# Kernel tuning notes

Hardware: AMD Instinct MI355X
Metric: run time of the kernel (lower is better)

## Reference

```python
import jax, jax.numpy as jnp
import numpy as np

B, L, D, K, MAXL = 2, 1024, 256, 64, 1024
EPS = 1e-5

def _encode(x, pos, w1, b1, w2, b2, wa, ba):
    # x: [B,L,D] -> complex phasors [B,L,K]
    xa = x + pos[: x.shape[1]][None]
    h = jax.nn.gelu(xa @ w1 + b1, approximate=False)
    phase = jnp.tanh(h @ w2 + b2) * np.float32(np.pi)
    amp = jax.nn.softplus(xa @ wa + ba) + np.float32(0.1)
    return (amp * jnp.exp(1j * phase)).astype(jnp.complex64)

def setup_inputs() -> dict:
    key = jax.random.key(0)
    ks = jax.random.split(key, 24)
    def lin_w(k, i, o):
        return (jax.random.normal(k, (i, o), jnp.float32) / np.sqrt(np.float32(i)))
    def pos(k):
        return jax.random.normal(k, (MAXL, D), jnp.float32) * np.float32(0.02)
    inp = {
        'x': jax.random.normal(ks[0], (B, L, D), jnp.float32),
        'pos_k': pos(ks[1]),
        'w1_k': lin_w(ks[2], D, D), 'b1_k': jnp.zeros((D,), jnp.float32),
        'w2_k': lin_w(ks[3], D, K), 'b2_k': jnp.zeros((K,), jnp.float32),
        'wa_k': lin_w(ks[4], D, K), 'ba_k': jnp.zeros((K,), jnp.float32),
        'pos_q': pos(ks[5]),
        'w1_q': lin_w(ks[6], D, D), 'b1_q': jnp.zeros((D,), jnp.float32),
        'w2_q': lin_w(ks[7], D, K), 'b2_q': jnp.zeros((K,), jnp.float32),
        'wa_q': lin_w(ks[8], D, K), 'ba_q': jnp.zeros((K,), jnp.float32),
        'wv': lin_w(ks[9], D, D), 'bv': jnp.zeros((D,), jnp.float32),
        'ln_g': jnp.ones((D,), jnp.float32), 'ln_b': jnp.zeros((D,), jnp.float32),
        'wo': lin_w(ks[10], D, D), 'bo': jnp.zeros((D,), jnp.float32),
    }
    return inp

def reference(x, pos_k, w1_k, b1_k, w2_k, b2_k, wa_k, ba_k,
              pos_q, w1_q, b1_q, w2_q, b2_q, wa_q, ba_q,
              wv, bv, ln_g, ln_b, wo, bo):
    Bx, Lx, Dx = x.shape
    kp = _encode(x, pos_k, w1_k, b1_k, w2_k, b2_k, wa_k, ba_k)  # [B,L,K] complex
    qp = _encode(x, pos_q, w1_q, b1_q, w2_q, b2_q, wa_q, ba_q)  # [B,L,K] complex
    V = (x @ wv + bv).astype(jnp.complex64)                      # [B,L,D]
    bound = kp[:, :, :, None] * V[:, :, None, :]                 # [B,L,K,D]
    memory = jnp.cumsum(bound, axis=1)                           # [B,L,K,D]
    retrieved = jnp.real(jnp.einsum('blkd,blk->bld', memory, jnp.conj(qp)))
    positions = jnp.arange(1, Lx + 1, dtype=jnp.float32)
    norm = jnp.sqrt(positions * np.float32(kp.shape[-1]))[None, :, None]
    r = retrieved / norm
    mu = jnp.mean(r, axis=-1, keepdims=True)
    var = jnp.var(r, axis=-1, keepdims=True)
    rn = (r - mu) / jnp.sqrt(var + np.float32(EPS)) * ln_g + ln_b
    return x + rn @ wo + bo
```

## Files before the change

### kernel.cpp

```cpp
#include <hip/hip_runtime.h>
#include <hip/hip_bf16.h>

typedef __attribute__((ext_vector_type(8))) short short8;
typedef __attribute__((ext_vector_type(4))) float float4v;

constexpr int B = 2, L = 1024, D = 256, K = 64;
constexpr int N = B * L;
constexpr int NC = L / 64;

constexpr int WT2_OFF = 524288;

__device__ __forceinline__ ushort bf16_hi(float v) {
  return (ushort)(__float_as_uint(v) >> 16);
}
__device__ __forceinline__ float hi_f(float v) {
  return __uint_as_float(__float_as_uint(v) & 0xFFFF0000u);
}
__device__ __forceinline__ ushort bf16_rne(float v) {
  uint b = __float_as_uint(v);
  b += 0x7FFF + ((b >> 16) & 1);
  return (ushort)(b >> 16);
}

__global__ __launch_bounds__(256) void prep_kernel(
    const float* __restrict__ w1_k, const float* __restrict__ w1_q,
    const float* __restrict__ wv, const float* __restrict__ wo,
    const float* __restrict__ w2_k, const float* __restrict__ wa_k,
    const float* __restrict__ w2_q, const float* __restrict__ wa_q,
    ushort* __restrict__ WT) {
  __shared__ float Lt[64][65];
  const int bi = blockIdx.x, tid = threadIdx.x;
  const float* src;
  int ncols, k0, n0;
  ushort* dhi;
  int losz;
  if (bi < 64) {
    const int m = bi >> 4, t = bi & 15;
    src = (m == 0) ? w1_k : (m == 1) ? w1_q : (m == 2) ? wv : wo;
    ncols = 256; k0 = (t >> 2) * 64; n0 = (t & 3) * 64;
    dhi = WT + m * 131072; losz = 65536;
  } else {
    const int m = (bi - 64) >> 2, kt = (bi - 64) & 3;
    src = (m == 0) ? w2_k : (m == 1) ? wa_k : (m == 2) ? w2_q : wa_q;
    ncols = 64; k0 = kt * 64; n0 = 0;
    dhi = WT + WT2_OFF + m * 32768; losz = 16384;
  }
  ushort* dlo = dhi + losz;
  for (int p = 0; p < 16; ++p) {
    const int kr = p * 4 + (tid >> 6), nc = tid & 63;
    Lt[kr][nc] = src[(k0 + kr) * ncols + n0 + nc];
  }
  __syncthreads();
  const int n = tid >> 2, kq = tid & 3;
  uint uh[8], ul[8];
  for (int i = 0; i < 8; ++i) {
    const float v0 = Lt[kq * 16 + 2 * i][n];
    const float v1 = Lt[kq * 16 + 2 * i + 1][n];
    uh[i] = (uint)bf16_hi(v0) | ((uint)bf16_hi(v1) << 16);
    ul[i] = (uint)bf16_rne(v0 - hi_f(v0)) | ((uint)bf16_rne(v1 - hi_f(v1)) << 16);
  }
  const int oidx = (n0 + n) * 256 + k0 + kq * 16;
  *(uint4*)&dhi[oidx] = make_uint4(uh[0], uh[1], uh[2], uh[3]);
  *(uint4*)&dhi[oidx + 8] = make_uint4(uh[4], uh[5], uh[6], uh[7]);
  *(uint4*)&dlo[oidx] = make_uint4(ul[0], ul[1], ul[2], ul[3]);
  *(uint4*)&dlo[oidx + 8] = make_uint4(ul[4], ul[5], ul[6], ul[7]);
}

__global__ __launch_bounds__(256) void enc1_kernel(
    const float* __restrict__ x, const float* __restrict__ pos_k,
    const float* __restrict__ pos_q,
    const float* __restrict__ b1_k, const float* __restrict__ b1_q,
    const float* __restrict__ bv, const ushort* __restrict__ WT,
    float* __restrict__ hk, float* __restrict__ hq, float* __restrict__ V) {
  __shared__ __align__(16) ushort Ah[32][40], Al[32][40];
  __shared__ __align__(16) ushort Bh[128][40], Bl[128][40];
  const int tid = threadIdx.x;
  const int g = blockIdx.x / 128;
  const int rem = blockIdx.x % 128;
  const int row0 = (rem >> 1) * 32, nb = (rem & 1) * 128;
  const float* pos = (g == 0) ? pos_k : (g == 1) ? pos_q : nullptr;
  const ushort* Wh = WT + g * 131072;
  const ushort* Wl = Wh + 65536;
  const int w = tid >> 6, lane = tid & 63;
  const int m16 = lane & 15, quad = lane >> 4;

  float4v acc[2][2] = {};

  for (int k0 = 0; k0 < 256; k0 += 32) {
    __syncthreads();
    {
      const int r = tid >> 3, kc = (tid & 7) * 4;
      const int row = row0 + r, l = row & (L - 1);
      float4 xv = *(const float4*)&x[row * D + k0 + kc];
      if (pos) {
        const float4 pv = *(const float4*)&pos[l * D + k0 + kc];
        xv.x += pv.x; xv.y += pv.y; xv.z += pv.z; xv.w += pv.w;
      }
      ushort4 h4, l4;
      h4.x = bf16_hi(xv.x); l4.x = bf16_rne(xv.x - hi_f(xv.x));
      h4.y = bf16_hi(xv.y); l4.y = bf16_rne(xv.y - hi_f(xv.y));
      h4.z = bf16_hi(xv.z); l4.z = bf16_rne(xv.z - hi_f(xv.z));
      h4.w = bf16_hi(xv.w); l4.w = bf16_rne(xv.w - hi_f(xv.w));
      *(ushort4*)&Ah[r][kc] = h4;
      *(ushort4*)&Al[r][kc] = l4;
    }
#pragma unroll
    for (int p = 0; p < 2; ++p) {
      const int n = (tid >> 2) + p * 64, chunk = tid & 3;
      const int ga = (nb + n) * 256 + k0 + chunk * 8;
      *(uint4*)&Bh[n][chunk * 8] = *(const uint4*)&Wh[ga];
      *(uint4*)&Bl[n][chunk * 8] = *(const uint4*)&Wl[ga];
    }
    __syncthreads();

    short8 afh[2], afl[2], bfh[2], bfl[2];
#pragma unroll
    for (int r = 0; r < 2; ++r) {
      afh[r] = *(const short8*)&Ah[r * 16 + m16][quad * 8];
      afl[r] = *(const short8*)&Al[r * 16 + m16][quad * 8];
    }
#pragma unroll
    for (int c = 0; c < 2; ++c) {
      const int col = w * 32 + c * 16 + m16;
      bfh[c] = *(const short8*)&Bh[col][quad * 8];
      bfl[c] = *(const short8*)&Bl[col][quad * 8];
    }
#pragma unroll
    for (int r = 0; r < 2; ++r)
#pragma unroll
      for (int c = 0; c < 2; ++c) {
        acc[r][c] = __builtin_amdgcn_mfma_f32_16x16x32_bf16(afh[r], bfh[c], acc[r][c], 0, 0, 0);
        acc[r][c] = __builtin_amdgcn_mfma_f32_16x16x32_bf16(afh[r], bfl[c], acc[r][c], 0, 0, 0);
        acc[r][c] = __builtin_amdgcn_mfma_f32_16x16x32_bf16(afl[r], bfh[c], acc[r][c], 0, 0, 0);
      }
  }

  float* outp = (g == 0) ? hk : (g == 1) ? hq : V;
  const float* bp = (g == 0) ? b1_k : (g == 1) ? b1_q : bv;
#pragma unroll
  for (int c = 0; c < 2; ++c) {
    const int colg = nb + w * 32 + c * 16 + m16;
    const float bias = bp[colg];
#pragma unroll
    for (int r = 0; r < 2; ++r)
#pragma unroll
      for (int j = 0; j < 4; ++j) {
        const int rowg = row0 + r * 16 + quad * 4 + j;
        float v = acc[r][c][j] + bias;
        if (g < 2) v = 0.5f * v * (1.0f + erff(v * 0.70710678f));
        outp[rowg * D + colg] = v;
      }
  }
}

__global__ __launch_bounds__(256) void enc2_kernel(
    const float* __restrict__ x, const float* __restrict__ pos_k,
    const float* __restrict__ pos_q, const float* __restrict__ hk,
    const float* __restrict__ hq,
    const float* __restrict__ b2_k, const float* __restrict__ ba_k,
    const float* __restrict__ b2_q, const float* __restrict__ ba_q,
    const ushort* __restrict__ WT,
    float* __restrict__ kr, float* __restrict__ ki,
    float* __restrict__ qr, float* __restrict__ qi) {
  __shared__ __align__(16) ushort Ahh[16][40], Ahl[16][40], Axh[16][40], Axl[16][40];
  __shared__ __align__(16) ushort B2h[64][40], B2l[64][40], Bah[64][40], Bal[64][40];
  const int tid = threadIdx.x;
  const int e = blockIdx.x >> 7;
  const int r0g = (blockIdx.x & 127) * 16;
  const float* hsrc = e ? hq : hk;
  const float* pos = e ? pos_q : pos_k;
  const ushort* W2h = WT + WT2_OFF + (e ? 2 : 0) * 32768;
  const ushort* W2l = W2h + 16384;
  const ushort* Wah = WT + WT2_OFF + (e ? 3 : 1) * 32768;
  const ushort* Wal = Wah + 16384;
  const int w = tid >> 6, lane = tid & 63;
  const int m16 = lane & 15, quad = lane >> 4;

  float4v accP = {}, accA = {};
  for (int k0 = 0; k0 < 256; k0 += 32) {
    __syncthreads();
    {
      const int r = tid >> 4, kc = (tid & 15) * 2;
      const int row = r0g + r, l = row & (L - 1);
      const float2 hv = *(const float2*)&hsrc[row * D + k0 + kc];
      const float2 xv = *(const float2*)&x[row * D + k0 + kc];
      const float2 pv = *(const float2*)&pos[l * D + k0 + kc];
      const float a0 = xv.x + pv.x, a1 = xv.y + pv.y;
      ushort2 t;
      t.x = bf16_hi(hv.x); t.y = bf16_hi(hv.y); *(ushort2*)&Ahh[r][kc] = t;
      t.x = bf16_rne(hv.x - hi_f(hv.x)); t.y = bf16_rne(hv.y - hi_f(hv.y));
      *(ushort2*)&Ahl[r][kc] = t;
      t.x = bf16_hi(a0); t.y = bf16_hi(a1); *(ushort2*)&Axh[r][kc] = t;
      t.x = bf16_rne(a0 - hi_f(a0)); t.y = bf16_rne(a1 - hi_f(a1));
      *(ushort2*)&Axl[r][kc] = t;
    }
    {
      const int n = tid >> 2, chunk = tid & 3;
      const int ga = n * 256 + k0 + chunk * 8;
      *(uint4*)&B2h[n][chunk * 8] = *(const uint4*)&W2h[ga];
      *(uint4*)&B2l[n][chunk * 8] = *(const uint4*)&W2l[ga];
      *(uint4*)&Bah[n][chunk * 8] = *(const uint4*)&Wah[ga];
      *(uint4*)&Bal[n][chunk * 8] = *(const uint4*)&Wal[ga];
    }
    __syncthreads();

    const short8 ahh = *(const short8*)&Ahh[m16][quad * 8];
    const short8 ahl = *(const short8*)&Ahl[m16][quad * 8];
    const short8 axh = *(const short8*)&Axh[m16][quad * 8];
    const short8 axl = *(const short8*)&Axl[m16][quad * 8];
    const int col = w * 16 + m16;
    const short8 b2h = *(const short8*)&B2h[col][quad * 8];
    const short8 b2l = *(const short8*)&B2l[col][quad * 8];
    const short8 bah = *(const short8*)&Bah[col][quad * 8];
    const short8 bal = *(const short8*)&Bal[col][quad * 8];
    accP = __builtin_amdgcn_mfma_f32_16x16x32_bf16(ahh, b2h, accP, 0, 0, 0);
    accP = __builtin_amdgcn_mfma_f32_16x16x32_bf16(ahh, b2l, accP, 0, 0, 0);
    accP = __builtin_amdgcn_mfma_f32_16x16x32_bf16(ahl, b2h, accP, 0, 0, 0);
    accA = __builtin_amdgcn_mfma_f32_16x16x32_bf16(axh, bah, accA, 0, 0, 0);
    accA = __builtin_amdgcn_mfma_f32_16x16x32_bf16(axh, bal, accA, 0, 0, 0);
    accA = __builtin_amdgcn_mfma_f32_16x16x32_bf16(axl, bah, accA, 0, 0, 0);
  }

  float* pr = e ? qr : kr;
  float* pim = e ? qi : ki;
  const float* b2 = e ? b2_q : b2_k;
  const float* ba = e ? ba_q : ba_k;
  const int colk = w * 16 + m16;
  const float b2v = b2[colk], bav = ba[colk];
#pragma unroll
  for (int j = 0; j < 4; ++j) {
    const int row = r0g + quad * 4 + j;
    const float ph = tanhf(accP[j] + b2v) * 3.14159265358979f;
    const float av = accA[j] + bav;
    const float am = fmaxf(av, 0.0f) + log1pf(expf(-fabsf(av))) + 0.1f;
    pr[row * K + colk] = am * cosf(ph);
    pim[row * K + colk] = am * sinf(ph);
  }
}

__global__ __launch_bounds__(256) void tbuild_kernel(
    const float* __restrict__ kr, const float* __restrict__ ki,
    const float* __restrict__ V, float* __restrict__ TMt) {
  const int id = blockIdx.x;
  const int dc = id & 15, c = (id >> 4) & 15, b = id >> 8;
  const int tid = threadIdx.x;
  const int n0 = b * L + c * 64;
  const int dl = tid & 15;
  const int d = dc * 16 + dl;
  const int kb = tid >> 4;

  __shared__ float krL[64][68], kiL[64][68];
  __shared__ float Tl[16][200];
  for (int e = tid; e < 1024; e += 256) {
    const int t = e >> 4, k4 = (e & 15) * 4;
    *(float4*)&krL[t][k4] = *(const float4*)&kr[(n0 + t) * K + k4];
    *(float4*)&kiL[t][k4] = *(const float4*)&ki[(n0 + t) * K + k4];
  }
  __syncthreads();

  float vcol[64];
#pragma unroll 8
  for (int t = 0; t < 64; ++t) vcol[t] = V[(n0 + t) * D + d];

  float ar[4] = {0.f, 0.f, 0.f, 0.f}, ai[4] = {0.f, 0.f, 0.f, 0.f};
#pragma unroll 4
  for (int t = 0; t < 64; ++t) {
    const float vt = vcol[t];
    const float4 k4r = *(const float4*)&krL[t][kb * 4];
    const float4 k4i = *(const float4*)&kiL[t][kb * 4];
    ar[0] += k4r.x * vt; ar[1] += k4r.y * vt; ar[2] += k4r.z * vt; ar[3] += k4r.w * vt;
    ai[0] += k4i.x * vt; ai[1] += k4i.y * vt; ai[2] += k4i.z * vt; ai[3] += k4i.w * vt;
  }

#pragma unroll
  for (int i = 0; i < 4; ++i) {
    Tl[dl][kb * 4 + i] = ar[i];
    Tl[dl][64 + kb * 4 + i] = ai[i];
  }
  if (kb == 0) {
#pragma unroll
    for (int j = 0; j < 16; ++j) Tl[dl][128 + j] = vcol[j];
  } else if (kb == 1) {
#pragma unroll
    for (int j = 0; j < 16; ++j) Tl[dl][144 + j] = vcol[16 + j];
  } else if (kb == 2) {
#pragma unroll
    for (int j = 0; j < 16; ++j) Tl[dl][160 + j] = vcol[32 + j];
  } else if (kb == 3) {
#pragma unroll
    for (int j = 0; j < 16; ++j) Tl[dl][176 + j] = vcol[48 + j];
  }
  __syncthreads();

  float* dst = &TMt[(((size_t)(b * 16 + c)) * 256 + dc * 16) * 192];
#pragma unroll
  for (int p = 0; p < 3; ++p) {
    const int e = p * 256 + tid;
    const int row = e / 48, f4 = e % 48;
    *(float4*)&dst[(size_t)row * 192 + f4 * 4] = *(const float4*)&Tl[row][f4 * 4];
  }
}

__global__ __launch_bounds__(256) void scan_kernel(float* __restrict__ TMt) {
  const int col = blockIdx.x * 256 + threadIdx.x;
  const int b = col >> 15;
  const int d = (col >> 7) & 255;
  const int inner = col & 127;
  size_t idx = (((size_t)(b * 16)) * 256 + d) * 192 + inner;
  const size_t stride = (size_t)256 * 192;
  float run = 0.f;
#pragma unroll
  for (int c = 0; c < NC; ++c, idx += stride) {
    const float t = TMt[idx];
    TMt[idx] = run;
    run += t;
  }
}

__global__ __launch_bounds__(256) void ret_kernel(
    const float* __restrict__ qr, const float* __restrict__ qi,
    const float* __restrict__ kr, const float* __restrict__ ki,
    const float* __restrict__ TMt, float* __restrict__ ret,
    float* __restrict__ LNred) {
  __shared__ __align__(16) ushort Ah[64][200], Al[64][200];
  __shared__ __align__(16) ushort Kh[64][136], Kl[64][136];
  __shared__ __align__(16) ushort Bh[32][200], Bl[32][200];
  const int tid = threadIdx.x;
  const int dc = blockIdx.x & 7;
  const int c = (blockIdx.x >> 3) & 15;
  const int b = blockIdx.x >> 7;
  const int n0 = b * L + c * 64;
  const int cols0 = dc * 32;
  const int w = tid >> 6, lane = tid & 63;
  const int m16 = lane & 15, quad = lane >> 4;

#pragma unroll
  for (int j = 0; j < 8; ++j) {
    const int e = j * 256 + tid;
    const int row = e >> 5, c4 = e & 31;
    const int col0 = (c4 & 15) * 4;
    const int acol = (c4 < 16 ? 0 : 64) + col0;
    {
      const float* src = (c4 < 16) ? qr : qi;
      const float4 v = *(const float4*)&src[(n0 + row) * K + col0];
      ushort4 h4, l4;
      h4.x = bf16_hi(v.x); l4.x = bf16_rne(v.x - hi_f(v.x));
      h4.y = bf16_hi(v.y); l4.y = bf16_rne(v.y - hi_f(v.y));
      h4.z = bf16_hi(v.z); l4.z = bf16_rne(v.z - hi_f(v.z));
      h4.w = bf16_hi(v.w); l4.w = bf16_rne(v.w - hi_f(v.w));
      *(ushort4*)&Ah[row][acol] = h4;
      *(ushort4*)&Al[row][acol] = l4;
    }
    {
      const float* src = (c4 < 16) ? kr : ki;
      const float4 v = *(const float4*)&src[(n0 + row) * K + col0];
      ushort4 h4, l4;
      h4.x = bf16_hi(v.x); l4.x = bf16_rne(v.x - hi_f(v.x));
      h4.y = bf16_hi(v.y); l4.y = bf16_rne(v.y - hi_f(v.y));
      h4.z = bf16_hi(v.z); l4.z = bf16_rne(v.z - hi_f(v.z));
      h4.w = bf16_hi(v.w); l4.w = bf16_rne(v.w - hi_f(v.w));
      *(ushort4*)&Kh[row][acol] = h4;
      *(ushort4*)&Kl[row][acol] = l4;
    }
  }
  __syncthreads();

  {
    float4v sc[4] = {};
#pragma unroll
    for (int kk = 0; kk < 128; kk += 32) {
      const short8 ah = *(const short8*)&Ah[w * 16 + m16][kk + quad * 8];
      const short8 al = *(const short8*)&Al[w * 16 + m16][kk + quad * 8];
#pragma unroll
      for (int ct = 0; ct < 4; ++ct) {
        const short8 bh = *(const short8*)&Kh[ct * 16 + m16][kk + quad * 8];
        const short8 bl = *(const short8*)&Kl[ct * 16 + m16][kk + quad * 8];
        sc[ct] = __builtin_amdgcn_mfma_f32_16x16x32_bf16(ah, bh, sc[ct], 0, 0, 0);
        sc[ct] = __builtin_amdgcn_mfma_f32_16x16x32_bf16(ah, bl, sc[ct], 0, 0, 0);
        sc[ct] = __builtin_amdgcn_mfma_f32_16x16x32_bf16(al, bh, sc[ct], 0, 0, 0);
      }
    }
#pragma unroll
    for (int ct = 0; ct < 4; ++ct)
#pragma unroll
      for (int j = 0; j < 4; ++j) {
        const int row = w * 16 + quad * 4 + j;
        const int t = ct * 16 + m16;
        const float s = (t <= row) ? sc[ct][j] : 0.0f;
        Ah[row][128 + t] = bf16_hi(s);
        Al[row][128 + t] = bf16_rne(s - hi_f(s));
      }
  }

  {
    const float* src = &TMt[(((size_t)(b * 16 + c)) * 256 + cols0) * 192];
#pragma unroll
    for (int p = 0; p < 6; ++p) {
      const int e = p * 256 + tid;
      const int row = e / 48, f4 = e % 48;
      const float4 v = *(const float4*)&src[(size_t)row * 192 + f4 * 4];
      ushort4 h4, l4;
      h4.x = bf16_hi(v.x); l4.x = bf16_rne(v.x - hi_f(v.x));
      h4.y = bf16_hi(v.y); l4.y = bf16_rne(v.y - hi_f(v.y));
      h4.z = bf16_hi(v.z); l4.z = bf16_rne(v.z - hi_f(v.z));
      h4.w = bf16_hi(v.w); l4.w = bf16_rne(v.w - hi_f(v.w));
      *(ushort4*)&Bh[row][f4 * 4] = h4;
      *(ushort4*)&Bl[row][f4 * 4] = l4;
    }
  }
  __syncthreads();

  {
    float4v r2[2] = {};
#pragma unroll
    for (int kk = 0; kk < 6; ++kk) {
      const short8 ah = *(const short8*)&Ah[w * 16 + m16][kk * 32 + quad * 8];
      const short8 al = *(const short8*)&Al[w * 16 + m16][kk * 32 + quad * 8];
#pragma unroll
      for (int ct = 0; ct < 2; ++ct) {
        const short8 bh = *(const short8*)&Bh[ct * 16 + m16][kk * 32 + quad * 8];
        const short8 bl = *(const short8*)&Bl[ct * 16 + m16][kk * 32 + quad * 8];
        r2[ct] = __builtin_amdgcn_mfma_f32_16x16x32_bf16(ah, bh, r2[ct], 0, 0, 0);
        r2[ct] = __builtin_amdgcn_mfma_f32_16x16x32_bf16(ah, bl, r2[ct], 0, 0, 0);
        r2[ct] = __builtin_amdgcn_mfma_f32_16x16x32_bf16(al, bh, r2[ct], 0, 0, 0);
      }
    }
#pragma unroll
    for (int j = 0; j < 4; ++j) {
      const int rowL = w * 16 + quad * 4 + j;
      const float nrm = rsqrtf((float)(c * 64 + rowL + 1) * 64.0f);
      float sj = 0.f, s2j = 0.f;
#pragma unroll
      for (int ct = 0; ct < 2; ++ct) {
        const float v = r2[ct][j] * nrm;
        ret[(size_t)(n0 + rowL) * D + cols0 + ct * 16 + m16] = v;
        sj += v; s2j += v * v;
      }
      for (int off = 1; off < 16; off <<= 1) {
        sj += __shfl_xor(sj, off, 64);
        s2j += __shfl_xor(s2j, off, 64);
      }
      if (m16 == 0) {
        LNred[(size_t)(n0 + rowL) * 16 + dc * 2 + 0] = sj;
        LNred[(size_t)(n0 + rowL) * 16 + dc * 2 + 1] = s2j;
      }
    }
  }
}

__global__ __launch_bounds__(256) void out2_kernel(
    const float* __restrict__ ret, const float* __restrict__ LNred,
    const float* __restrict__ x, const float* __restrict__ ln_g,
    const float* __restrict__ ln_b, const ushort* __restrict__ WT,
    const float* __restrict__ bo, float* __restrict__ out) {
  __shared__ __align__(16) ushort Ah[32][40], Al[32][40];
  __shared__ __align__(16) ushort Bh[64][40], Bl[64][40];
  __shared__ float mu_s[32], rs_s[32];
  const int tid = threadIdx.x;
  const int row0 = (blockIdx.x >> 2) * 32, nb = (blockIdx.x & 3) * 64;
  const ushort* Wh = WT + 3 * 131072;
  const ushort* Wl = Wh + 65536;
  const int w = tid >> 6, lane = tid & 63;
  const int m16 = lane & 15, quad = lane >> 4;

  if (tid < 32) {
    const int row = row0 + tid;
    float s = 0.f, s2 = 0.f;
#pragma unroll
    for (int i = 0; i < 8; ++i) {
      s += LNred[(size_t)row * 16 + i * 2 + 0];
      s2 += LNred[(size_t)row * 16 + i * 2 + 1];
    }
    const float mu = s * (1.0f / 256.0f);
    mu_s[tid] = mu;
    rs_s[tid] = rsqrtf(s2 * (1.0f / 256.0f) - mu * mu + 1e-5f);
  }

  float4v acc[2] = {};
  for (int k0 = 0; k0 < 256; k0 += 32) {
    __syncthreads();
    {
      const int r = tid >> 3, kc = (tid & 7) * 4;
      const float4 v = *(const float4*)&ret[(size_t)(row0 + r) * D + k0 + kc];
      const float4 g4 = *(const float4*)&ln_g[k0 + kc];
      const float4 b4 = *(const float4*)&ln_b[k0 + kc];
      const float mu = mu_s[r], rs = rs_s[r];
      float a0 = (v.x - mu) * rs * g4.x + b4.x;
      float a1 = (v.y - mu) * rs * g4.y + b4.y;
      float a2 = (v.z - mu) * rs * g4.z + b4.z;
      float a3 = (v.w - mu) * rs * g4.w + b4.w;
      ushort4 h4, l4;
      h4.x = bf16_hi(a0); l4.x = bf16_rne(a0 - hi_f(a0));
      h4.y = bf16_hi(a1); l4.y = bf16_rne(a1 - hi_f(a1));
      h4.z = bf16_hi(a2); l4.z = bf16_rne(a2 - hi_f(a2));
      h4.w = bf16_hi(a3); l4.w = bf16_rne(a3 - hi_f(a3));
      *(ushort4*)&Ah[r][kc] = h4;
      *(ushort4*)&Al[r][kc] = l4;
    }
    {
      const int n = tid >> 2, chunk = tid & 3;
      const int ga = (nb + n) * 256 + k0 + chunk * 8;
      *(uint4*)&Bh[n][chunk * 8] = *(const uint4*)&Wh[ga];
      *(uint4*)&Bl[n][chunk * 8] = *(const uint4*)&Wl[ga];
    }
    __syncthreads();

    short8 afh[2], afl[2];
#pragma unroll
    for (int r = 0; r < 2; ++r) {
      afh[r] = *(const short8*)&Ah[r * 16 + m16][quad * 8];
      afl[r] = *(const short8*)&Al[r * 16 + m16][quad * 8];
    }
    const int col = w * 16 + m16;
    const short8 bfh = *(const short8*)&Bh[col][quad * 8];
    const short8 bfl = *(const short8*)&Bl[col][quad * 8];
#pragma unroll
    for (int r = 0; r < 2; ++r) {
      acc[r] = __builtin_amdgcn_mfma_f32_16x16x32_bf16(afh[r], bfh, acc[r], 0, 0, 0);
      acc[r] = __builtin_amdgcn_mfma_f32_16x16x32_bf16(afh[r], bfl, acc[r], 0, 0, 0);
      acc[r] = __builtin_amdgcn_mfma_f32_16x16x32_bf16(afl[r], bfh, acc[r], 0, 0, 0);
    }
  }

  const int colg = nb + w * 16 + m16;
  const float bias = bo[colg];
#pragma unroll
  for (int r = 0; r < 2; ++r)
#pragma unroll
    for (int j = 0; j < 4; ++j) {
      const int rowg = row0 + r * 16 + quad * 4 + j;
      out[rowg * D + colg] = x[rowg * D + colg] + acc[r][j] + bias;
    }
}

extern "C" void kernel_launch(void* const* d_in, const int* in_sizes, int n_in,
                              void* d_out, int out_size, void* d_ws, size_t ws_size,
                              hipStream_t stream) {
  (void)in_sizes; (void)n_in; (void)out_size; (void)ws_size;
  const float* x    = (const float*)d_in[0];
  const float* pos_k= (const float*)d_in[1];
  const float* w1_k = (const float*)d_in[2];
  const float* b1_k = (const float*)d_in[3];
  const float* w2_k = (const float*)d_in[4];
  const float* b2_k = (const float*)d_in[5];
  const float* wa_k = (const float*)d_in[6];
  const float* ba_k = (const float*)d_in[7];
  const float* pos_q= (const float*)d_in[8];
  const float* w1_q = (const float*)d_in[9];
  const float* b1_q = (const float*)d_in[10];
  const float* w2_q = (const float*)d_in[11];
  const float* b2_q = (const float*)d_in[12];
  const float* wa_q = (const float*)d_in[13];
  const float* ba_q = (const float*)d_in[14];
  const float* wv   = (const float*)d_in[15];
  const float* bv   = (const float*)d_in[16];
  const float* ln_g = (const float*)d_in[17];
  const float* ln_b = (const float*)d_in[18];
  const float* wo   = (const float*)d_in[19];
  const float* bo   = (const float*)d_in[20];

  float* ws = (float*)d_ws;
  float* kr = ws;
  float* ki = kr + (size_t)N * K;
  float* qr = ki + (size_t)N * K;
  float* qi = qr + (size_t)N * K;
  float* V  = qi + (size_t)N * K;
  float* TMt = V + (size_t)N * D;
  float* ret = TMt + (size_t)B * NC * 256 * 192;
  float* LNred = ret + (size_t)N * D;
  float* hk = LNred + (size_t)N * 16;
  float* hq = hk + (size_t)N * D;
  ushort* WT = (ushort*)(hq + (size_t)N * D);

  prep_kernel<<<80, 256, 0, stream>>>(w1_k, w1_q, wv, wo,
                                      w2_k, wa_k, w2_q, wa_q, WT);
  enc1_kernel<<<384, 256, 0, stream>>>(x, pos_k, pos_q, b1_k, b1_q, bv, WT,
                                       hk, hq, V);
  enc2_kernel<<<256, 256, 0, stream>>>(x, pos_k, pos_q, hk, hq,
                                       b2_k, ba_k, b2_q, ba_q, WT,
                                       kr, ki, qr, qi);
  tbuild_kernel<<<B * NC * 16, 256, 0, stream>>>(kr, ki, V, TMt);
  scan_kernel<<<256, 256, 0, stream>>>(TMt);
  ret_kernel<<<B * NC * 8, 256, 0, stream>>>(qr, qi, kr, ki, TMt, ret, LNred);
  out2_kernel<<<256, 256, 0, stream>>>(ret, LNred, x, ln_g, ln_b, WT, bo,
                                       (float*)d_out);
}
```

Before: 160.9 us.

## Double block size to 512 threads in enc2, ret, and out2 kernels

```diff
diff --git a/kernel.cpp b/kernel.cpp
--- a/kernel.cpp
+++ b/kernel.cpp
@@ -153,7 +153,7 @@
   }
 }
 
-__global__ __launch_bounds__(256) void enc2_kernel(
+__global__ __launch_bounds__(512) void enc2_kernel(
     const float* __restrict__ x, const float* __restrict__ pos_k,
     const float* __restrict__ pos_q, const float* __restrict__ hk,
     const float* __restrict__ hq,
@@ -164,6 +164,7 @@
     float* __restrict__ qr, float* __restrict__ qi) {
   __shared__ __align__(16) ushort Ahh[16][40], Ahl[16][40], Axh[16][40], Axl[16][40];
   __shared__ __align__(16) ushort B2h[64][40], B2l[64][40], Bah[64][40], Bal[64][40];
+  __shared__ float phL[16][68], amL[16][68];
   const int tid = threadIdx.x;
   const int e = blockIdx.x >> 7;
   const int r0g = (blockIdx.x & 127) * 16;
@@ -175,66 +176,90 @@
   const ushort* Wal = Wah + 16384;
   const int w = tid >> 6, lane = tid & 63;
   const int m16 = lane & 15, quad = lane >> 4;
-
-  float4v accP = {}, accA = {};
+  const int mat = w & 1, ct = w >> 1;
+
+  float4v acc = {};
   for (int k0 = 0; k0 < 256; k0 += 32) {
     __syncthreads();
     {
-      const int r = tid >> 4, kc = (tid & 15) * 2;
+      const int half = tid >> 8;
+      const int t2 = tid & 255;
+      const int r = t2 >> 4, kc = (t2 & 15) * 2;
       const int row = r0g + r, l = row & (L - 1);
-      const float2 hv = *(const float2*)&hsrc[row * D + k0 + kc];
-      const float2 xv = *(const float2*)&x[row * D + k0 + kc];
-      const float2 pv = *(const float2*)&pos[l * D + k0 + kc];
-      const float a0 = xv.x + pv.x, a1 = xv.y + pv.y;
-      ushort2 t;
-      t.x = bf16_hi(hv.x); t.y = bf16_hi(hv.y); *(ushort2*)&Ahh[r][kc] = t;
-      t.x = bf16_rne(hv.x - hi_f(hv.x)); t.y = bf16_rne(hv.y - hi_f(hv.y));
-      *(ushort2*)&Ahl[r][kc] = t;
-      t.x = bf16_hi(a0); t.y = bf16_hi(a1); *(ushort2*)&Axh[r][kc] = t;
-      t.x = bf16_rne(a0 - hi_f(a0)); t.y = bf16_rne(a1 - hi_f(a1));
-      *(ushort2*)&Axl[r][kc] = t;
-    }
-    {
-      const int n = tid >> 2, chunk = tid & 3;
-      const int ga = n * 256 + k0 + chunk * 8;
-      *(uint4*)&B2h[n][chunk * 8] = *(const uint4*)&W2h[ga];
-      *(uint4*)&B2l[n][chunk * 8] = *(const uint4*)&W2l[ga];
-      *(uint4*)&Bah[n][chunk * 8] = *(const uint4*)&Wah[ga];
-      *(uint4*)&Bal[n][chunk * 8] = *(const uint4*)&Wal[ga];
+      if (half == 0) {
+        const float2 hv = *(const float2*)&hsrc[row * D + k0 + kc];
+        ushort2 h2, l2;
+        h2.x = bf16_hi(hv.x); l2.x = bf16_rne(hv.x - hi_f(hv.x));
+        h2.y = bf16_hi(hv.y); l2.y = bf16_rne(hv.y - hi_f(hv.y));
+        *(ushort2*)&Ahh[r][kc] = h2;
+        *(ushort2*)&Ahl[r][kc] = l2;
+      } else {
+        const float2 xv = *(const float2*)&x[row * D + k0 + kc];
+        const float2 pv = *(const float2*)&pos[l * D + k0 + kc];
+        const float a0 = xv.x + pv.x, a1 = xv.y + pv.y;
+        ushort2 h2, l2;
+        h2.x = bf16_hi(a0); l2.x = bf16_rne(a0 - hi_f(a0));
+        h2.y = bf16_hi(a1); l2.y = bf16_rne(a1 - hi_f(a1));
+        *(ushort2*)&Axh[r][kc] = h2;
+        *(ushort2*)&Axl[r][kc] = l2;
+      }
+    }
+    {
+      const int sel = tid >> 7;
+      const int idx = tid & 127;
+      const int n = idx >> 1, ch = (idx & 1) * 2;
+      const int ga = n * 256 + k0 + ch * 8;
+      const ushort* s = (sel == 0) ? W2h : (sel == 1) ? W2l : (sel == 2) ? Wah : Wal;
+      ushort* dst = (sel == 0) ? &B2h[n][ch * 8] : (sel == 1) ? &B2l[n][ch * 8]
+                  : (sel == 2) ? &Bah[n][ch * 8] : &Bal[n][ch * 8];
+      *(uint4*)dst = *(const uint4*)&s[ga];
+      *(uint4*)(dst + 8) = *(const uint4*)&s[ga + 8];
     }
     __syncthreads();
 
-    const short8 ahh = *(const short8*)&Ahh[m16][quad * 8];
-    const short8 ahl = *(const short8*)&Ahl[m16][quad * 8];
-    const short8 axh = *(const short8*)&Axh[m16][quad * 8];
-    const short8 axl = *(const short8*)&Axl[m16][quad * 8];
-    const int col = w * 16 + m16;
-    const short8 b2h = *(const short8*)&B2h[col][quad * 8];
-    const short8 b2l = *(const short8*)&B2l[col][quad * 8];
-    const short8 bah = *(const short8*)&Bah[col][quad * 8];
-    const short8 bal = *(const short8*)&Bal[col][quad * 8];
-    accP = __builtin_amdgcn_mfma_f32_16x16x32_bf16(ahh, b2h, accP, 0, 0, 0);
-    accP = __builtin_amdgcn_mfma_f32_16x16x32_bf16(ahh, b2l, accP, 0, 0, 0);
-    accP = __builtin_amdgcn_mfma_f32_16x16x32_bf16(ahl, b2h, accP, 0, 0, 0);
-    accA = __builtin_amdgcn_mfma_f32_16x16x32_bf16(axh, bah, accA, 0, 0, 0);
-    accA = __builtin_amdgcn_mfma_f32_16x16x32_bf16(axh, bal, accA, 0, 0, 0);
-    accA = __builtin_amdgcn_mfma_f32_16x16x32_bf16(axl, bah, accA, 0, 0, 0);
-  }
-
-  float* pr = e ? qr : kr;
-  float* pim = e ? qi : ki;
-  const float* b2 = e ? b2_q : b2_k;
-  const float* ba = e ? ba_q : ba_k;
-  const int colk = w * 16 + m16;
-  const float b2v = b2[colk], bav = ba[colk];
-#pragma unroll
-  for (int j = 0; j < 4; ++j) {
-    const int row = r0g + quad * 4 + j;
-    const float ph = tanhf(accP[j] + b2v) * 3.14159265358979f;
-    const float av = accA[j] + bav;
-    const float am = fmaxf(av, 0.0f) + log1pf(expf(-fabsf(av))) + 0.1f;
-    pr[row * K + colk] = am * cosf(ph);
-    pim[row * K + colk] = am * sinf(ph);
+    const short8 ah = mat ? *(const short8*)&Axh[m16][quad * 8]
+                          : *(const short8*)&Ahh[m16][quad * 8];
+    const short8 al = mat ? *(const short8*)&Axl[m16][quad * 8]
+                          : *(const short8*)&Ahl[m16][quad * 8];
+    const int col = ct * 16 + m16;
+    const short8 bh = mat ? *(const short8*)&Bah[col][quad * 8]
+                          : *(const short8*)&B2h[col][quad * 8];
+    const short8 bl = mat ? *(const short8*)&Bal[col][quad * 8]
+                          : *(const short8*)&B2l[col][quad * 8];
+    acc = __builtin_amdgcn_mfma_f32_16x16x32_bf16(ah, bh, acc, 0, 0, 0);
+    acc = __builtin_amdgcn_mfma_f32_16x16x32_bf16(ah, bl, acc, 0, 0, 0);
+    acc = __builtin_amdgcn_mfma_f32_16x16x32_bf16(al, bh, acc, 0, 0, 0);
+  }
+
+  {
+    const int colk = ct * 16 + m16;
+    if (mat == 0) {
+      const float b2v = (e ? b2_q : b2_k)[colk];
+#pragma unroll
+      for (int j = 0; j < 4; ++j)
+        phL[quad * 4 + j][colk] = tanhf(acc[j] + b2v) * 3.14159265358979f;
+    } else {
+      const float bav = (e ? ba_q : ba_k)[colk];
+#pragma unroll
+      for (int j = 0; j < 4; ++j) {
+        const float av = acc[j] + bav;
+        amL[quad * 4 + j][colk] = fmaxf(av, 0.0f) + log1pf(expf(-fabsf(av))) + 0.1f;
+      }
+    }
+  }
+  __syncthreads();
+  {
+    float* pr = e ? qr : kr;
+    float* pim = e ? qi : ki;
+#pragma unroll
+    for (int p = 0; p < 2; ++p) {
+      const int idx = p * 512 + tid;
+      const int r = idx >> 6, ccol = idx & 63;
+      const int row = r0g + r;
+      const float a = amL[r][ccol], pph = phL[r][ccol];
+      pr[row * K + ccol] = a * cosf(pph);
+      pim[row * K + ccol] = a * sinf(pph);
+    }
   }
 }
 
@@ -317,7 +342,7 @@
   }
 }
 
-__global__ __launch_bounds__(256) void ret_kernel(
+__global__ __launch_bounds__(512) void ret_kernel(
     const float* __restrict__ qr, const float* __restrict__ qi,
     const float* __restrict__ kr, const float* __restrict__ ki,
     const float* __restrict__ TMt, float* __restrict__ ret,
@@ -335,8 +360,8 @@
   const int m16 = lane & 15, quad = lane >> 4;
 
 #pragma unroll
-  for (int j = 0; j < 8; ++j) {
-    const int e = j * 256 + tid;
+  for (int j = 0; j < 4; ++j) {
+    const int e = j * 512 + tid;
     const int row = e >> 5, c4 = e & 31;
     const int col0 = (c4 & 15) * 4;
     const int acol = (c4 < 16 ? 0 : 64) + col0;
@@ -366,27 +391,30 @@
   __syncthreads();
 
   {
-    float4v sc[4] = {};
+    const int rt = w & 3;
+    const int cp = (w >> 2) * 2;
+    float4v sc[2] = {};
 #pragma unroll
     for (int kk = 0; kk < 128; kk += 32) {
-      const short8 ah = *(const short8*)&Ah[w * 16 + m16][kk + quad * 8];
-      const short8 al = *(const short8*)&Al[w * 16 + m16][kk + quad * 8];
-#pragma unroll
-      for (int ct = 0; ct < 4; ++ct) {
+      const short8 ah = *(const short8*)&Ah[rt * 16 + m16][kk + quad * 8];
+      const short8 al = *(const short8*)&Al[rt * 16 + m16][kk + quad * 8];
+#pragma unroll
+      for (int cc = 0; cc < 2; ++cc) {
+        const int ct = cp + cc;
         const short8 bh = *(const short8*)&Kh[ct * 16 + m16][kk + quad * 8];
         const short8 bl = *(const short8*)&Kl[ct * 16 + m16][kk + quad * 8];
-        sc[ct] = __builtin_amdgcn_mfma_f32_16x16x32_bf16(ah, bh, sc[ct], 0, 0, 0);
-        sc[ct] = __builtin_amdgcn_mfma_f32_16x16x32_bf16(ah, bl, sc[ct], 0, 0, 0);
-        sc[ct] = __builtin_amdgcn_mfma_f32_16x16x32_bf16(al, bh, sc[ct], 0, 0, 0);
-      }
-    }
-#pragma unroll
-    for (int ct = 0; ct < 4; ++ct)
+        sc[cc] = __builtin_amdgcn_mfma_f32_16x16x32_bf16(ah, bh, sc[cc], 0, 0, 0);
+        sc[cc] = __builtin_amdgcn_mfma_f32_16x16x32_bf16(ah, bl, sc[cc], 0, 0, 0);
+        sc[cc] = __builtin_amdgcn_mfma_f32_16x16x32_bf16(al, bh, sc[cc], 0, 0, 0);
+      }
+    }
+#pragma unroll
+    for (int cc = 0; cc < 2; ++cc)
 #pragma unroll
       for (int j = 0; j < 4; ++j) {
-        const int row = w * 16 + quad * 4 + j;
-        const int t = ct * 16 + m16;
-        const float s = (t <= row) ? sc[ct][j] : 0.0f;
+        const int row = rt * 16 + quad * 4 + j;
+        const int t = (cp + cc) * 16 + m16;
+        const float s = (t <= row) ? sc[cc][j] : 0.0f;
         Ah[row][128 + t] = bf16_hi(s);
         Al[row][128 + t] = bf16_rne(s - hi_f(s));
       }
@@ -395,8 +423,8 @@
   {
     const float* src = &TMt[(((size_t)(b * 16 + c)) * 256 + cols0) * 192];
 #pragma unroll
-    for (int p = 0; p < 6; ++p) {
-      const int e = p * 256 + tid;
+    for (int p = 0; p < 3; ++p) {
+      const int e = p * 512 + tid;
       const int row = e / 48, f4 = e % 48;
       const float4 v = *(const float4*)&src[(size_t)row * 192 + f4 * 4];
       ushort4 h4, l4;
@@ -411,44 +439,39 @@
   __syncthreads();
 
   {
-    float4v r2[2] = {};
+    const int rt = w & 3;
+    const int ct = w >> 2;
+    float4v r2 = {};
 #pragma unroll
     for (int kk = 0; kk < 6; ++kk) {
-      const short8 ah = *(const short8*)&Ah[w * 16 + m16][kk * 32 + quad * 8];
-      const short8 al = *(const short8*)&Al[w * 16 + m16][kk * 32 + quad * 8];
-#pragma unroll
-      for (int ct = 0; ct < 2; ++ct) {
-        const short8 bh = *(const short8*)&Bh[ct * 16 + m16][kk * 32 + quad * 8];
-        const short8 bl = *(const short8*)&Bl[ct * 16 + m16][kk * 32 + quad * 8];
-        r2[ct] = __builtin_amdgcn_mfma_f32_16x16x32_bf16(ah, bh, r2[ct], 0, 0, 0);
-        r2[ct] = __builtin_amdgcn_mfma_f32_16x16x32_bf16(ah, bl, r2[ct], 0, 0, 0);
-        r2[ct] = __builtin_amdgcn_mfma_f32_16x16x32_bf16(al, bh, r2[ct], 0, 0, 0);
-      }
+      const short8 ah = *(const short8*)&Ah[rt * 16 + m16][kk * 32 + quad * 8];
+      const short8 al = *(const short8*)&Al[rt * 16 + m16][kk * 32 + quad * 8];
+      const short8 bh = *(const short8*)&Bh[ct * 16 + m16][kk * 32 + quad * 8];
+      const short8 bl = *(const short8*)&Bl[ct * 16 + m16][kk * 32 + quad * 8];
+      r2 = __builtin_amdgcn_mfma_f32_16x16x32_bf16(ah, bh, r2, 0, 0, 0);
+      r2 = __builtin_amdgcn_mfma_f32_16x16x32_bf16(ah, bl, r2, 0, 0, 0);
+      r2 = __builtin_amdgcn_mfma_f32_16x16x32_bf16(al, bh, r2, 0, 0, 0);
     }
 #pragma unroll
     for (int j = 0; j < 4; ++j) {
-      const int rowL = w * 16 + quad * 4 + j;
+      const int rowL = rt * 16 + quad * 4 + j;
       const float nrm = rsqrtf((float)(c * 64 + rowL + 1) * 64.0f);
-      float sj = 0.f, s2j = 0.f;
-#pragma unroll
-      for (int ct = 0; ct < 2; ++ct) {
-        const float v = r2[ct][j] * nrm;
-        ret[(size_t)(n0 + rowL) * D + cols0 + ct * 16 + m16] = v;
-        sj += v; s2j += v * v;
-      }
+      const float v = r2[j] * nrm;
+      ret[(size_t)(n0 + rowL) * D + cols0 + ct * 16 + m16] = v;
+      float sj = v, s2j = v * v;
       for (int off = 1; off < 16; off <<= 1) {
         sj += __shfl_xor(sj, off, 64);
         s2j += __shfl_xor(s2j, off, 64);
       }
       if (m16 == 0) {
-        LNred[(size_t)(n0 + rowL) * 16 + dc * 2 + 0] = sj;
-        LNred[(size_t)(n0 + rowL) * 16 + dc * 2 + 1] = s2j;
-      }
-    }
-  }
-}
-
-__global__ __launch_bounds__(256) void out2_kernel(
+        LNred[(size_t)(n0 + rowL) * 32 + (dc * 2 + ct) * 2 + 0] = sj;
+        LNred[(size_t)(n0 + rowL) * 32 + (dc * 2 + ct) * 2 + 1] = s2j;
+      }
+    }
+  }
+}
+
+__global__ __launch_bounds__(512) void out2_kernel(
     const float* __restrict__ ret, const float* __restrict__ LNred,
     const float* __restrict__ x, const float* __restrict__ ln_g,
     const float* __restrict__ ln_b, const ushort* __restrict__ WT,
@@ -462,75 +485,64 @@
   const ushort* Wl = Wh + 65536;
   const int w = tid >> 6, lane = tid & 63;
   const int m16 = lane & 15, quad = lane >> 4;
+  const int rt = w & 1, cq = w >> 1;
 
   if (tid < 32) {
     const int row = row0 + tid;
     float s = 0.f, s2 = 0.f;
 #pragma unroll
-    for (int i = 0; i < 8; ++i) {
-      s += LNred[(size_t)row * 16 + i * 2 + 0];
-      s2 += LNred[(size_t)row * 16 + i * 2 + 1];
+    for (int i = 0; i < 16; ++i) {
+      s += LNred[(size_t)row * 32 + i * 2 + 0];
+      s2 += LNred[(size_t)row * 32 + i * 2 + 1];
     }
     const float mu = s * (1.0f / 256.0f);
     mu_s[tid] = mu;
     rs_s[tid] = rsqrtf(s2 * (1.0f / 256.0f) - mu * mu + 1e-5f);
   }
 
-  float4v acc[2] = {};
+  float4v acc = {};
   for (int k0 = 0; k0 < 256; k0 += 32) {
     __syncthreads();
     {
-      const int r = tid >> 3, kc = (tid & 7) * 4;
-      const float4 v = *(const float4*)&ret[(size_t)(row0 + r) * D + k0 + kc];
-      const float4 g4 = *(const float4*)&ln_g[k0 + kc];
-      const float4 b4 = *(const float4*)&ln_b[k0 + kc];
+      const int r = tid >> 4, kc = (tid & 15) * 2;
+      const float2 v = *(const float2*)&ret[(size_t)(row0 + r) * D + k0 + kc];
+      const float2 g2 = *(const float2*)&ln_g[k0 + kc];
+      const float2 b2 = *(const float2*)&ln_b[k0 + kc];
       const float mu = mu_s[r], rs = rs_s[r];
-      float a0 = (v.x - mu) * rs * g4.x + b4.x;
-      float a1 = (v.y - mu) * rs * g4.y + b4.y;
-      float a2 = (v.z - mu) * rs * g4.z + b4.z;
-      float a3 = (v.w - mu) * rs * g4.w + b4.w;
-      ushort4 h4, l4;
-      h4.x = bf16_hi(a0); l4.x = bf16_rne(a0 - hi_f(a0));
-      h4.y = bf16_hi(a1); l4.y = bf16_rne(a1 - hi_f(a1));
-      h4.z = bf16_hi(a2); l4.z = bf16_rne(a2 - hi_f(a2));
-      h4.w = bf16_hi(a3); l4.w = bf16_rne(a3 - hi_f(a3));
-      *(ushort4*)&Ah[r][kc] = h4;
-      *(ushort4*)&Al[r][kc] = l4;
-    }
-    {
-      const int n = tid >> 2, chunk = tid & 3;
+      const float a0 = (v.x - mu) * rs * g2.x + b2.x;
+      const float a1 = (v.y - mu) * rs * g2.y + b2.y;
+      ushort2 h2, l2;
+      h2.x = bf16_hi(a0); l2.x = bf16_rne(a0 - hi_f(a0));
+      h2.y = bf16_hi(a1); l2.y = bf16_rne(a1 - hi_f(a1));
+      *(ushort2*)&Ah[r][kc] = h2;
+      *(ushort2*)&Al[r][kc] = l2;
+    }
+    {
+      const int plane = tid >> 8;
+      const int n = (tid >> 2) & 63, chunk = tid & 3;
       const int ga = (nb + n) * 256 + k0 + chunk * 8;
-      *(uint4*)&Bh[n][chunk * 8] = *(const uint4*)&Wh[ga];
-      *(uint4*)&Bl[n][chunk * 8] = *(const uint4*)&Wl[ga];
+      if (plane == 0) *(uint4*)&Bh[n][chunk * 8] = *(const uint4*)&Wh[ga];
+      else            *(uint4*)&Bl[n][chunk * 8] = *(const uint4*)&Wl[ga];
     }
     __syncthreads();
 
-    short8 afh[2], afl[2];
-#pragma unroll
-    for (int r = 0; r < 2; ++r) {
-      afh[r] = *(const short8*)&Ah[r * 16 + m16][quad * 8];
-      afl[r] = *(const short8*)&Al[r * 16 + m16][quad * 8];
-    }
-    const int col = w * 16 + m16;
+    const short8 afh = *(const short8*)&Ah[rt * 16 + m16][quad * 8];
+    const short8 afl = *(const short8*)&Al[rt * 16 + m16][quad * 8];
+    const int col = cq * 16 + m16;
     const short8 bfh = *(const short8*)&Bh[col][quad * 8];
     const short8 bfl = *(const short8*)&Bl[col][quad * 8];
-#pragma unroll
-    for (int r = 0; r < 2; ++r) {
-      acc[r] = __builtin_amdgcn_mfma_f32_16x16x32_bf16(afh[r], bfh, acc[r], 0, 0, 0);
-      acc[r] = __builtin_amdgcn_mfma_f32_16x16x32_bf16(afh[r], bfl, acc[r], 0, 0, 0);
-      acc[r] = __builtin_amdgcn_mfma_f32_16x16x32_bf16(afl[r], bfh, acc[r], 0, 0, 0);
-    }
-  }
-
-  const int colg = nb + w * 16 + m16;
+    acc = __builtin_amdgcn_mfma_f32_16x16x32_bf16(afh, bfh, acc, 0, 0, 0);
+    acc = __builtin_amdgcn_mfma_f32_16x16x32_bf16(afh, bfl, acc, 0, 0, 0);
+    acc = __builtin_amdgcn_mfma_f32_16x16x32_bf16(afl, bfh, acc, 0, 0, 0);
+  }
+
+  const int colg = nb + cq * 16 + m16;
   const float bias = bo[colg];
 #pragma unroll
-  for (int r = 0; r < 2; ++r)
-#pragma unroll
-    for (int j = 0; j < 4; ++j) {
-      const int rowg = row0 + r * 16 + quad * 4 + j;
-      out[rowg * D + colg] = x[rowg * D + colg] + acc[r][j] + bias;
-    }
+  for (int j = 0; j < 4; ++j) {
+    const int rowg = row0 + rt * 16 + quad * 4 + j;
+    out[rowg * D + colg] = x[rowg * D + colg] + acc[j] + bias;
+  }
 }
 
 extern "C" void kernel_launch(void* const* d_in, const int* in_sizes, int n_in,
@@ -568,7 +580,7 @@
   float* TMt = V + (size_t)N * D;
   float* ret = TMt + (size_t)B * NC * 256 * 192;
   float* LNred = ret + (size_t)N * D;
-  float* hk = LNred + (size_t)N * 16;
+  float* hk = LNred + (size_t)N * 32;
   float* hq = hk + (size_t)N * D;
   ushort* WT = (ushort*)(hq + (size_t)N * D);
 
@@ -576,12 +588,12 @@
                                       w2_k, wa_k, w2_q, wa_q, WT);
   enc1_kernel<<<384, 256, 0, stream>>>(x, pos_k, pos_q, b1_k, b1_q, bv, WT,
                                        hk, hq, V);
-  enc2_kernel<<<256, 256, 0, stream>>>(x, pos_k, pos_q, hk, hq,
+  enc2_kernel<<<256, 512, 0, stream>>>(x, pos_k, pos_q, hk, hq,
                                        b2_k, ba_k, b2_q, ba_q, WT,
                                        kr, ki, qr, qi);
   tbuild_kernel<<<B * NC * 16, 256, 0, stream>>>(kr, ki, V, TMt);
   scan_kernel<<<256, 256, 0, stream>>>(TMt);
-  ret_kernel<<<B * NC * 8, 256, 0, stream>>>(qr, qi, kr, ki, TMt, ret, LNred);
-  out2_kernel<<<256, 256, 0, stream>>>(ret, LNred, x, ln_g, ln_b, WT, bo,
+  ret_kernel<<<B * NC * 8, 512, 0, stream>>>(qr, qi, kr, ki, TMt, ret, LNred);
+  out2_kernel<<<256, 512, 0, stream>>>(ret, LNred, x, ln_g, ln_b, WT, bo,
                                        (float*)d_out);
 }
```

New measurement: 160.2 us. Within noise of the previous version (-0.4%).
